# Performance work log

Measured on AMD Instinct MI355X. Metric: run time of the kernel, lower is better.

Reference implementation:

```python
import jax, jax.numpy as jnp
import numpy as np

B, H, W = 16, 512, 512


def _nmax(a, pad_val):
    """Max over 3x3 cross (4-neighborhood + center), constant-padded borders."""
    p = jnp.pad(a, ((0, 0), (1, 1), (1, 1)), constant_values=pad_val)
    return jnp.maximum(a, jnp.maximum(
        jnp.maximum(p[:, :-2, 1:-1], p[:, 2:, 1:-1]),
        jnp.maximum(p[:, 1:-1, :-2], p[:, 1:-1, 2:])))


def _dilate(b):
    # cv2 dilate with 3x3 MORPH_ELLIPSE (== cross), border treated as background
    return _nmax(b, 0.0)


def _erode(b):
    # cv2 erode default border value == foreground, so erode = 1 - dilate(1 - b)
    return 1.0 - _nmax(1.0 - b, 0.0)


def setup_inputs() -> dict:
    key = jax.random.key(0)
    x = jax.random.uniform(key, (B, 4, H, W), dtype=jnp.float32)
    return {"x": x}


def reference(x):
    # --- majority vote with disagreement fallback to pred1 ---
    p1 = (x[:, 1] > 0.5).astype(jnp.float32)
    p2 = (x[:, 2] > 0.5).astype(jnp.float32)
    p3 = (x[:, 3] > 0.5).astype(jnp.float32)
    vote = p1 + p2 + p3
    m = jnp.where(vote >= 2, 1.0, jnp.where(vote == 1, p1, 0.0))

    # --- morphology: MORPH_CLOSE then MORPH_OPEN with 3x3 ellipse (cross) ---
    m = _erode(_dilate(m))   # close
    m = _dilate(_erode(m))   # open

    # --- 4-connected CCL (scipy ndimage.label default) via label propagation ---
    Bm, Hm, Wm = m.shape
    mask_i = m > 0
    init = jnp.where(mask_i,
                     jnp.arange(1, Hm * Wm + 1, dtype=jnp.int32).reshape(1, Hm, Wm),
                     jnp.int32(0))

    def cond(s):
        return s[1]

    def body(s):
        lbl, _ = s
        new = jnp.where(mask_i, _nmax(lbl, 0), 0)
        return (new, jnp.any(new != lbl))

    lbl, _ = jax.lax.while_loop(cond, body, (init, jnp.array(True)))

    # --- component sizes and small-component removal ---
    sizes = jax.vmap(lambda mm, ll: jax.ops.segment_sum(
        mm.ravel(), ll.ravel(), num_segments=Hm * Wm + 1))(m, lbl)
    min_size = max(50, int(0.001 * Hm * Wm))  # = 262 for 512x512
    keep = jnp.take_along_axis(sizes, lbl.reshape(Bm, -1), axis=1)
    keep = (keep.reshape(Bm, Hm, Wm) > min_size).astype(jnp.float32)
    m = m * keep
    return m[:, None, :, :]  # [B, 1, H, W]
```

## Files before the change

### kernel.cpp

```cpp
#include <hip/hip_runtime.h>

typedef unsigned long long u64;
typedef unsigned u32;

#define BATCH 16
#define Hh 512
#define Ww 512
#define IMG (Hh * Ww)
#define TOT (BATCH * IMG)
#define WPI 4096
#define WROW 8
#define NWORDS (TOT / 64)
#define MIN_SIZE 262
#define LHASH 2048
#define MAXRUNS (NWORDS * 32)

#define BAND 8
#define HALO 4
#define BROWS (BAND + 2 * HALO)
#define BWORDS (BROWS * WROW)
#define NODES (BAND * Ww)

__device__ __forceinline__ u32 runstart(u64 bits, int s) {
    u64 ms = (s >= 63) ? ~0ULL : ((1ULL << (s + 1)) - 1);
    u64 nz = ~bits & ms;
    return nz ? (u32)(64 - __clzll(nz)) : 0u;
}
__device__ __forceinline__ u32 runlen(u64 bits, int s) {
    u64 v = ~(bits >> s);
    return v ? (u32)(__ffsll(v) - 1) : (u32)(64 - s);
}

__device__ __forceinline__ u64 morph_word(const u64* M, int w, int rr, bool er) {
    const u64 B = er ? ~0ULL : 0ULL;
    int wx = w & 7;
    u64 cc = M[w];
    u64 lf = (cc << 1) | (wx > 0 ? (M[w - 1] >> 63) : (er ? 1ULL : 0ULL));
    u64 rt = (cc >> 1) | (wx < 7 ? (M[w + 1] << 63) : (er ? (1ULL << 63) : 0ULL));
    u64 up = (rr <= 0)      ? B : (w >= WROW          ? M[w - WROW] : B);
    u64 dn = (rr >= Hh - 1) ? B : (w < BWORDS - WROW  ? M[w + WROW] : B);
    return er ? (cc & lf & rt & up & dn) : (cc | lf | rt | up | dn);
}

template <typename P>
__device__ __forceinline__ u32 uf_find_halve(P L, u32 x) {
    while (true) {
        u32 p = L[x];
        if (p == x) return x;
        u32 gp = L[p];
        if (gp == p) return p;
        atomicMin(&L[x], gp);
        x = gp;
    }
}
template <typename P>
__device__ __forceinline__ void uf_merge(P L, u32 a, u32 b) {
    while (true) {
        a = uf_find_halve(L, a);
        b = uf_find_halve(L, b);
        if (a == b) return;
        if (a > b) { u32 t = a; a = b; b = t; }
        u32 old = atomicMin(&L[b], a);
        if (old == b) return;
        b = old;
    }
}

__global__ __launch_bounds__(256) void vote_pack_kernel(const float4* __restrict__ x4,
                                                        u64* __restrict__ mp0,
                                                        u32* __restrict__ runCtr) {
    int t = threadIdx.x, blk = blockIdx.x;
    if (blk == 0 && t == 0) *runCtr = 0u;
    int img = blk >> 6;
    size_t p4 = (size_t)((blk & 63) * 4096 + t * 16) >> 2;
    const float4* c1 = x4 + ((size_t)img * 4 + 1) * (IMG / 4);
    const float4* c2 = x4 + ((size_t)img * 4 + 2) * (IMG / 4);
    const float4* c3 = x4 + ((size_t)img * 4 + 3) * (IMG / 4);
    u32 m = 0;
    #pragma unroll
    for (int q = 0; q < 4; ++q) {
        float4 a1 = c1[p4 + q], a2 = c2[p4 + q], a3 = c3[p4 + q];
        u32 b0 = (a1.x > 0.5f) | ((a2.x > 0.5f) & (a3.x > 0.5f));
        u32 b1 = (a1.y > 0.5f) | ((a2.y > 0.5f) & (a3.y > 0.5f));
        u32 b2 = (a1.z > 0.5f) | ((a2.z > 0.5f) & (a3.z > 0.5f));
        u32 b3 = (a1.w > 0.5f) | ((a2.w > 0.5f) & (a3.w > 0.5f));
        m |= (b0 | (b1 << 1) | (b2 << 2) | (b3 << 3)) << (q * 4);
    }
    u32 w32 = m | (__shfl_xor(m, 1) << 16);
    u64 w = (u64)w32 | ((u64)__shfl_xor(w32, 2) << 32);
    if ((t & 3) == 0) mp0[(size_t)blk * 64 + (t >> 2)] = w;
}

__global__ __launch_bounds__(256) void morph_ccl_kernel(const u64* __restrict__ mp0,
                                                        u64* __restrict__ mp,
                                                        u32* __restrict__ L,
                                                        u32* __restrict__ wordbase,
                                                        u32* __restrict__ counts,
                                                        u32* __restrict__ runCtr) {
    __shared__ u64 Ma[BWORDS], Mb[BWORDS];
    __shared__ u32 Ll[NODES];
    __shared__ u32 wb_l[64];
    __shared__ u32 baseSh, totSh;
    int blk = blockIdx.x;
    int img = blk >> 6;
    int r0  = (blk & 63) * BAND;
    int t = threadIdx.x;
    int rr = r0 - HALO + (t >> 3);

    if (t < BWORDS)
        Ma[t] = (rr >= 0 && rr < Hh) ? mp0[(size_t)img * WPI + (size_t)rr * WROW + (t & 7)] : 0;
    for (int i = t; i < NODES; i += 256) Ll[i] = (u32)i;
    __syncthreads();

    if (t < BWORDS) Mb[t] = morph_word(Ma, t, rr, false);
    __syncthreads();
    if (t < BWORDS) Ma[t] = morph_word(Mb, t, rr, true);
    __syncthreads();
    if (t < BWORDS) Mb[t] = morph_word(Ma, t, rr, true);
    __syncthreads();
    if (t < BWORDS) Ma[t] = morph_word(Mb, t, rr, false);
    __syncthreads();

    if (t < 64)
        mp[(size_t)img * WPI + (size_t)r0 * WROW + t] = Ma[32 + t];

    u32 myexcl = 0;
    if (t < 64) {
        u64 bits = Ma[32 + t];
        u64 st = bits & ~(bits << 1);
        u32 cnt = __popcll(st);
        u32 inc = cnt;
        #pragma unroll
        for (int d = 1; d < 64; d <<= 1) {
            u32 v = __shfl_up(inc, d);
            if (t >= d) inc += v;
        }
        myexcl = inc - cnt;
        if (t == 63) { baseSh = atomicAdd(runCtr, inc); totSh = inc; }
    }
    __syncthreads();
    u32 base = baseSh, tot = totSh;
    if (t < 64) {
        wb_l[t] = base + myexcl;
        wordbase[(size_t)img * WPI + (size_t)r0 * WROW + t] = base + myexcl;
    }
    for (u32 i = t; i < tot; i += 256) counts[base + i] = 0u;
    __syncthreads();

    if (t < 56) {
        int rp = t >> 3, w = t & 7;
        u64 a = Ma[32 + rp * 8 + w], b = Ma[32 + (rp + 1) * 8 + w];
        u64 ov = a & b, seg = ov & ~(ov << 1);
        while (seg) {
            int s = __ffsll(seg) - 1; seg &= seg - 1;
            uf_merge((u32*)Ll, (u32)(rp * Ww + w * 64) + runstart(a, s),
                               (u32)((rp + 1) * Ww + w * 64) + runstart(b, s));
        }
    } else if (t >= 64 && t < 120) {
        int ht = t - 64;
        int r = ht / 7, w = 1 + ht % 7;
        u64 a = Ma[32 + r * 8 + w - 1], b = Ma[32 + r * 8 + w];
        if ((a >> 63) & b & 1ULL)
            uf_merge((u32*)Ll, (u32)(r * Ww + (w - 1) * 64) + runstart(a, 63),
                               (u32)(r * Ww + w * 64));
    }
    __syncthreads();

    if (t < 64) {
        u64 bits = Ma[32 + t];
        u64 st = bits & ~(bits << 1);
        u32 myid = wb_l[t];
        while (st) {
            int s = __ffsll(st) - 1; st &= st - 1;
            u32 n = (u32)(t >> 3) * Ww + (u32)(t & 7) * 64 + (u32)s;
            u32 r = n, p = Ll[r];
            while (p != r) { r = p; p = Ll[r]; }
            u32 rrow = r >> 9, rcol = r & 511;
            u32 rw = rrow * 8 + (rcol >> 6);
            u64 rbits = Ma[32 + rw];
            u64 rst = rbits & ~(rbits << 1);
            u32 rid = wb_l[rw] + (u32)__popcll(rst & (((u64)1 << (rcol & 63)) - 1));
            L[myid++] = rid;
        }
    }
}

#define BITEMS (BATCH * 63 * WROW)
__global__ void border_merge_kernel(const u64* __restrict__ mp,
                                    const u32* __restrict__ wordbase, u32* L) {
    int e = blockIdx.x * blockDim.x + threadIdx.x;
    if (e >= BITEMS) return;
    int w = e & 7, k = (e >> 3) % 63 + 1, img = e / (63 * 8);
    int R = k * BAND;
    size_t wa_i = (size_t)img * WPI + (size_t)(R - 1) * WROW + w;
    size_t wb_i = (size_t)img * WPI + (size_t)R * WROW + w;
    u64 a = mp[wa_i], b = mp[wb_i];
    u64 ov = a & b, seg = ov & ~(ov << 1);
    if (!seg) return;
    u64 sta = a & ~(a << 1), stb = b & ~(b << 1);
    u32 wba = wordbase[wa_i], wbb = wordbase[wb_i];
    while (seg) {
        int s = __ffsll(seg) - 1; seg &= seg - 1;
        u32 ra = runstart(a, s), rb = runstart(b, s);
        u32 ida = wba + (u32)__popcll(sta & (((u64)1 << ra) - 1));
        u32 idb = wbb + (u32)__popcll(stb & (((u64)1 << rb) - 1));
        uf_merge(L, ida, idb);
    }
}

__global__ __launch_bounds__(256) void count_kernel(const u64* __restrict__ mp,
                                                    const u32* __restrict__ wordbase,
                                                    u32* __restrict__ L,
                                                    u32* __restrict__ counts) {
    __shared__ u32 keys[LHASH];
    __shared__ u32 vals[LHASH];
    int tid = threadIdx.x;
    for (int i = tid; i < LHASH; i += 256) { keys[i] = 0xFFFFFFFFu; vals[i] = 0u; }
    __syncthreads();

    int widx = blockIdx.x * 256 + tid;
    u64 bits = mp[widx];
    u64 st = bits & ~(bits << 1);
    u32 id = wordbase[widx];

    u32 r = 0, len = 0;
    bool pending = false;
    if (st) {
        int s = __ffsll(st) - 1; st &= st - 1;
        u32 rr = id, p = L[rr];
        while (p != rr) { rr = p; p = L[rr]; }
        L[id] = rr;
        r = rr; len = runlen(bits, s); id++; pending = true;
    }
    while (true) {
        u64 act = __ballot(pending);
        if (!act) break;
        int leader = __ffsll(act) - 1;
        u32 lr = __shfl(r, leader);
        bool mine = pending && (r == lr);
        u32 c = mine ? len : 0u;
        c += __shfl_xor(c, 32); c += __shfl_xor(c, 16); c += __shfl_xor(c, 8);
        c += __shfl_xor(c, 4);  c += __shfl_xor(c, 2);  c += __shfl_xor(c, 1);
        if ((tid & 63) == leader) {
            u32 h = (lr * 2654435761u) & (LHASH - 1);
            while (true) {
                u32 k = atomicCAS(&keys[h], 0xFFFFFFFFu, lr);
                if (k == 0xFFFFFFFFu || k == lr) { atomicAdd(&vals[h], c); break; }
                h = (h + 1) & (LHASH - 1);
            }
        }
        if (mine) {
            if (st) {
                int s = __ffsll(st) - 1; st &= st - 1;
                u32 rr = id, p = L[rr];
                while (p != rr) { rr = p; p = L[rr]; }
                L[id] = rr;
                r = rr; len = runlen(bits, s); id++;
            } else pending = false;
        }
    }
    __syncthreads();
    for (int i = tid; i < LHASH; i += 256)
        if (keys[i] != 0xFFFFFFFFu) atomicAdd(&counts[keys[i]], vals[i]);
}

__global__ __launch_bounds__(256) void final_kernel(const u64* __restrict__ mp,
                                                    const u32* __restrict__ wordbase,
                                                    const u32* __restrict__ L,
                                                    const u32* __restrict__ counts,
                                                    float* __restrict__ out) {
    __shared__ u64 km[256];
    int tid = threadIdx.x;
    int widx = blockIdx.x * 256 + tid;
    u64 bits = mp[widx];
    u64 st = bits & ~(bits << 1);
    u32 id = wordbase[widx];
    u64 keep = 0;
    while (st) {
        int s = __ffsll(st) - 1; st &= st - 1;
        u32 r = L[id++];
        if (counts[r] > MIN_SIZE) {
            u32 len = runlen(bits, s);
            keep |= (len == 64 ? ~0ULL : ((1ULL << len) - 1ULL)) << s;
        }
    }
    km[tid] = keep;
    __syncthreads();
    float4* o4 = (float4*)out + (size_t)blockIdx.x * 4096;
    for (int i = tid; i < 4096; i += 256) {
        u32 nib = (u32)(km[i >> 4] >> ((i & 15) * 4)) & 0xFu;
        o4[i] = make_float4(nib & 1u ? 1.f : 0.f, nib & 2u ? 1.f : 0.f,
                            nib & 4u ? 1.f : 0.f, nib & 8u ? 1.f : 0.f);
    }
}

extern "C" void kernel_launch(void* const* d_in, const int* in_sizes, int n_in,
                              void* d_out, int out_size, void* d_ws, size_t ws_size,
                              hipStream_t stream) {
    const float* x = (const float*)d_in[0];
    float* out = (float*)d_out;

    u64* mp0 = (u64*)d_ws;
    u64* mp  = mp0 + NWORDS;
    u32* wordbase = (u32*)(mp + NWORDS);
    u32* L      = wordbase + NWORDS;
    u32* counts = L + MAXRUNS;
    u32* runCtr = counts + MAXRUNS;

    const int block = 256;

    vote_pack_kernel<<<1024, block, 0, stream>>>((const float4*)x, mp0, runCtr);
    morph_ccl_kernel<<<BATCH * 64, block, 0, stream>>>(mp0, mp, L, wordbase, counts, runCtr);
    border_merge_kernel<<<(BITEMS + block - 1) / block, block, 0, stream>>>(mp, wordbase, L);
    count_kernel<<<NWORDS / block, block, 0, stream>>>(mp, wordbase, L, counts);
    final_kernel<<<NWORDS / block, block, 0, stream>>>(mp, wordbase, L, counts, out);
}
```

Measured before the change: 81.77 us.

## Count component sizes per run with a flat grid instead of per-word hashing

```diff
diff --git a/kernel.cpp b/kernel.cpp
--- a/kernel.cpp
+++ b/kernel.cpp
@@ -2,6 +2,7 @@
 
 typedef unsigned long long u64;
 typedef unsigned u32;
+typedef unsigned char u8;
 
 #define BATCH 16
 #define Hh 512
@@ -12,7 +13,6 @@
 #define WROW 8
 #define NWORDS (TOT / 64)
 #define MIN_SIZE 262
-#define LHASH 2048
 #define MAXRUNS (NWORDS * 32)
 
 #define BAND 8
@@ -96,6 +96,7 @@
                                                         u32* __restrict__ L,
                                                         u32* __restrict__ wordbase,
                                                         u32* __restrict__ counts,
+                                                        u8*  __restrict__ len8,
                                                         u32* __restrict__ runCtr) {
     __shared__ u64 Ma[BWORDS], Mb[BWORDS];
     __shared__ u32 Ll[NODES];
@@ -180,7 +181,9 @@
             u64 rbits = Ma[32 + rw];
             u64 rst = rbits & ~(rbits << 1);
             u32 rid = wb_l[rw] + (u32)__popcll(rst & (((u64)1 << (rcol & 63)) - 1));
-            L[myid++] = rid;
+            L[myid] = rid;
+            len8[myid] = (u8)runlen(bits, s);
+            myid++;
         }
     }
 }
@@ -208,60 +211,39 @@
     }
 }
 
-__global__ __launch_bounds__(256) void count_kernel(const u64* __restrict__ mp,
-                                                    const u32* __restrict__ wordbase,
-                                                    u32* __restrict__ L,
-                                                    u32* __restrict__ counts) {
-    __shared__ u32 keys[LHASH];
-    __shared__ u32 vals[LHASH];
+#define ACCUM_STRIDE (1024 * 256)
+__global__ __launch_bounds__(256) void accum_kernel(u32* __restrict__ L,
+                                                    const u8* __restrict__ len8,
+                                                    u32* __restrict__ counts,
+                                                    const u32* __restrict__ runCtr) {
+    u32 n = *runCtr;
+    u32 gid = blockIdx.x * 256 + threadIdx.x;
     int tid = threadIdx.x;
-    for (int i = tid; i < LHASH; i += 256) { keys[i] = 0xFFFFFFFFu; vals[i] = 0u; }
-    __syncthreads();
-
-    int widx = blockIdx.x * 256 + tid;
-    u64 bits = mp[widx];
-    u64 st = bits & ~(bits << 1);
-    u32 id = wordbase[widx];
-
-    u32 r = 0, len = 0;
-    bool pending = false;
-    if (st) {
-        int s = __ffsll(st) - 1; st &= st - 1;
-        u32 rr = id, p = L[rr];
-        while (p != rr) { rr = p; p = L[rr]; }
-        L[id] = rr;
-        r = rr; len = runlen(bits, s); id++; pending = true;
-    }
-    while (true) {
-        u64 act = __ballot(pending);
-        if (!act) break;
-        int leader = __ffsll(act) - 1;
-        u32 lr = __shfl(r, leader);
-        bool mine = pending && (r == lr);
-        u32 c = mine ? len : 0u;
-        c += __shfl_xor(c, 32); c += __shfl_xor(c, 16); c += __shfl_xor(c, 8);
-        c += __shfl_xor(c, 4);  c += __shfl_xor(c, 2);  c += __shfl_xor(c, 1);
-        if ((tid & 63) == leader) {
-            u32 h = (lr * 2654435761u) & (LHASH - 1);
-            while (true) {
-                u32 k = atomicCAS(&keys[h], 0xFFFFFFFFu, lr);
-                if (k == 0xFFFFFFFFu || k == lr) { atomicAdd(&vals[h], c); break; }
-                h = (h + 1) & (LHASH - 1);
-            }
-        }
-        if (mine) {
-            if (st) {
-                int s = __ffsll(st) - 1; st &= st - 1;
-                u32 rr = id, p = L[rr];
-                while (p != rr) { rr = p; p = L[rr]; }
-                L[id] = rr;
-                r = rr; len = runlen(bits, s); id++;
-            } else pending = false;
-        }
-    }
-    __syncthreads();
-    for (int i = tid; i < LHASH; i += 256)
-        if (keys[i] != 0xFFFFFFFFu) atomicAdd(&counts[keys[i]], vals[i]);
+    u32 trips = (n + ACCUM_STRIDE - 1) / ACCUM_STRIDE;
+    for (u32 k = 0; k < trips; ++k) {
+        u32 id = gid + k * ACCUM_STRIDE;
+        bool valid = id < n;
+        u32 r = 0xFFFFFFFFu, len = 0;
+        if (valid) {
+            r = id; u32 p = L[r];
+            while (p != r) { r = p; p = L[r]; }
+            L[id] = r;
+            len = len8[id];
+        }
+        bool pending = true;
+        while (true) {
+            u64 act = __ballot(pending);
+            if (!act) break;
+            int leader = __ffsll(act) - 1;
+            u32 lr = __shfl(r, leader);
+            bool mine = pending && (r == lr);
+            u32 c = mine ? len : 0u;
+            c += __shfl_xor(c, 32); c += __shfl_xor(c, 16); c += __shfl_xor(c, 8);
+            c += __shfl_xor(c, 4);  c += __shfl_xor(c, 2);  c += __shfl_xor(c, 1);
+            if ((tid & 63) == leader && lr != 0xFFFFFFFFu) atomicAdd(&counts[lr], c);
+            if (mine) pending = false;
+        }
+    }
 }
 
 __global__ __launch_bounds__(256) void final_kernel(const u64* __restrict__ mp,
@@ -305,13 +287,14 @@
     u32* wordbase = (u32*)(mp + NWORDS);
     u32* L      = wordbase + NWORDS;
     u32* counts = L + MAXRUNS;
-    u32* runCtr = counts + MAXRUNS;
+    u8*  len8   = (u8*)(counts + MAXRUNS);
+    u32* runCtr = (u32*)(len8 + MAXRUNS);
 
     const int block = 256;
 
     vote_pack_kernel<<<1024, block, 0, stream>>>((const float4*)x, mp0, runCtr);
-    morph_ccl_kernel<<<BATCH * 64, block, 0, stream>>>(mp0, mp, L, wordbase, counts, runCtr);
+    morph_ccl_kernel<<<BATCH * 64, block, 0, stream>>>(mp0, mp, L, wordbase, counts, len8, runCtr);
     border_merge_kernel<<<(BITEMS + block - 1) / block, block, 0, stream>>>(mp, wordbase, L);
-    count_kernel<<<NWORDS / block, block, 0, stream>>>(mp, wordbase, L, counts);
+    accum_kernel<<<1024, block, 0, stream>>>(L, len8, counts, runCtr);
     final_kernel<<<NWORDS / block, block, 0, stream>>>(mp, wordbase, L, counts, out);
 }
```

Measured after the change: 78.88 us. -3.5%, faster.
